# Kernel tuning notes

Measured on AMD Instinct MI355X. Metric: run time of the kernel, lower is better.

Reference implementation:

```python
import jax, jax.numpy as jnp
import numpy as np
from jax import lax

B, W_LEN, V, E, C, K, L = 8, 1000, 50000, 100, 50, 3, 18000


def setup_inputs() -> dict:
    key = jax.random.key(0)
    ks = jax.random.split(key, 7)
    return {
        "x": jax.random.randint(ks[0], (B, W_LEN), 0, V),
        "W_embed": jax.random.normal(ks[1], (V, E), dtype=jnp.float32) * 0.1,
        "conv_w": jax.random.normal(ks[2], (C, E, K), dtype=jnp.float32) * 0.08,
        "conv_b": jax.random.normal(ks[3], (C,), dtype=jnp.float32) * 0.01,
        "u_w": jax.random.normal(ks[4], (L, C), dtype=jnp.float32) * 0.1,
        "out_w": jax.random.normal(ks[5], (L, C), dtype=jnp.float32) * 0.1,
        "out_b": jax.random.normal(ks[6], (L,), dtype=jnp.float32) * 0.01,
    }


def reference(x, W_embed, conv_w, conv_b, u_w, out_w, out_b):
    # embedding lookup: (B, W, E)
    emb = W_embed[x]
    # conv1d over sequence, 'same' padding: (B, C, W)
    emb_ncw = jnp.transpose(emb, (0, 2, 1))
    H = lax.conv_general_dilated(
        emb_ncw, conv_w, window_strides=(1,), padding=[(K // 2, K // 2)],
        dimension_numbers=("NCH", "OIH", "NCH"))
    H = jnp.tanh(H + conv_b[None, :, None])
    H = jnp.transpose(H, (0, 2, 1))  # (B, W, C)
    # label-wise attention scores: (B, L, W), softmax over seq
    scores = jnp.einsum("lc,bwc->blw", u_w, H)
    attns = jax.nn.softmax(scores, axis=2)
    # attention-pooled reps: (B, L, C)
    m = jnp.einsum("blw,bwc->blc", attns, H)
    # per-label weighted dot product + bias, sigmoid: (B, L)
    out = jax.nn.sigmoid(jnp.sum(out_w[None] * m, axis=2) + out_b[None])
    return out
```

## Files before the change

### kernel.cpp

```cpp
#include <hip/hip_runtime.h>
#include <hip/hip_bf16.h>
#include <cmath>

#define AS1 __attribute__((address_space(1)))
#define AS3 __attribute__((address_space(3)))

#define B_ 8
#define W_LEN_ 1000
#define WP 1024
#define E_ 100
#define C_ 50
#define CPAD 64
#define HP 72
#define K_ 3
#define L_ 18000
#define TL 64
#define NLBLK ((L_ + TL - 1) / TL)
#define WTILE 128
#define CWT 16
#define NSLOT (K_ * (E_ / 4))

typedef __attribute__((ext_vector_type(8))) short bf16x8;
typedef __attribute__((ext_vector_type(4))) short bf16x4;
typedef __attribute__((ext_vector_type(4))) float f32x4;

static __device__ __forceinline__ void gl_lds16(const void* g, void* l) {
    __builtin_amdgcn_global_load_lds((const AS1 unsigned*)g, (AS3 unsigned*)l, 16, 0, 0);
}
static __device__ __forceinline__ float bf2f(short s) {
    return __uint_as_float(((unsigned)(unsigned short)s) << 16);
}

__global__ __launch_bounds__(256) void prep_all(
    const float* __restrict__ conv_w, const float* __restrict__ u_w,
    const float* __restrict__ out_w,
    bf16x4* __restrict__ cwTs, __hip_bfloat16* __restrict__ UO)
{
    int tid = blockIdx.x * blockDim.x + threadIdx.x;
    if (tid < NSLOT * C_) {
        int slot = tid / C_;
        int c    = tid % C_;
        int k = slot / (E_ / 4);
        int i = slot % (E_ / 4);
        bf16x4 v;
        #pragma unroll
        for (int q = 0; q < 4; q++) {
            __hip_bfloat16 h = __float2bfloat16(conv_w[((size_t)c * E_ + 4 * i + q) * K_ + k]);
            v[q] = *reinterpret_cast<short*>(&h);
        }
        cwTs[tid] = v;
    }
    if (tid < 2 * L_ * CPAD) {
        int c = tid & (CPAD - 1);
        int l = (tid >> 6) % L_;
        int m = tid / (L_ * CPAD);
        const float* src = m ? out_w : u_w;
        float v = (c < C_) ? src[(size_t)l * C_ + c] : 0.f;
        UO[tid] = __float2bfloat16(v);
    }
}

__global__ __launch_bounds__(256) void conv_kernel(
    const int* __restrict__ x,
    const float* __restrict__ W_embed,
    const bf16x4* __restrict__ cwTs,
    const float* __restrict__ conv_b,
    __hip_bfloat16* __restrict__ H)
{
    __shared__ float4 emb_s[(CWT + 2) * (E_ / 4)];
    __shared__ bf16x4 wS[NSLOT * C_];

    const int b  = blockIdx.y;
    const int w0 = blockIdx.x * CWT;
    const int tid = threadIdx.x;

    for (int i = tid; i < NSLOT * C_; i += 256) wS[i] = cwTs[i];

    for (int i = tid; i < (CWT + 2) * (E_ / 4); i += 256) {
        int row = i / (E_ / 4);
        int e4  = i % (E_ / 4);
        int ws  = w0 - 1 + row;
        float4 v = make_float4(0.f, 0.f, 0.f, 0.f);
        if ((unsigned)ws < (unsigned)W_LEN_)
            v = ((const float4*)(W_embed + (size_t)x[b * W_LEN_ + ws] * E_))[e4];
        emb_s[i] = v;
    }
    __syncthreads();

    const int c  = tid & 63;
    const int wq = tid >> 6;
    const int cc = (c < C_) ? c : 0;

    f32x4 acc[4];
    const float bias = conv_b[cc];
    #pragma unroll
    for (int j = 0; j < 4; j++) acc[j] = (f32x4){bias, 0.f, 0.f, 0.f};

    const float4* eb = &emb_s[wq * 4 * (E_ / 4)];

    #pragma unroll 5
    for (int i = 0; i < E_ / 4; i++) {
        bf16x4 kb0 = wS[i * C_ + cc];
        bf16x4 kb1 = wS[(25 + i) * C_ + cc];
        bf16x4 kb2 = wS[(50 + i) * C_ + cc];
        float4 k0 = make_float4(bf2f(kb0[0]), bf2f(kb0[1]), bf2f(kb0[2]), bf2f(kb0[3]));
        float4 k1 = make_float4(bf2f(kb1[0]), bf2f(kb1[1]), bf2f(kb1[2]), bf2f(kb1[3]));
        float4 k2 = make_float4(bf2f(kb2[0]), bf2f(kb2[1]), bf2f(kb2[2]), bf2f(kb2[3]));
        float4 e0 = eb[i],       e1 = eb[25 + i],  e2 = eb[50 + i];
        float4 e3 = eb[75 + i],  e4 = eb[100 + i], e5 = eb[125 + i];
        acc[0].x += e0.x*k0.x + e1.x*k1.x + e2.x*k2.x;
        acc[0].y += e0.y*k0.y + e1.y*k1.y + e2.y*k2.y;
        acc[0].z += e0.z*k0.z + e1.z*k1.z + e2.z*k2.z;
        acc[0].w += e0.w*k0.w + e1.w*k1.w + e2.w*k2.w;
        acc[1].x += e1.x*k0.x + e2.x*k1.x + e3.x*k2.x;
        acc[1].y += e1.y*k0.y + e2.y*k1.y + e3.y*k2.y;
        acc[1].z += e1.z*k0.z + e2.z*k1.z + e3.z*k2.z;
        acc[1].w += e1.w*k0.w + e2.w*k1.w + e3.w*k2.w;
        acc[2].x += e2.x*k0.x + e3.x*k1.x + e4.x*k2.x;
        acc[2].y += e2.y*k0.y + e3.y*k1.y + e4.y*k2.y;
        acc[2].z += e2.z*k0.z + e3.z*k1.z + e4.z*k2.z;
        acc[2].w += e2.w*k0.w + e3.w*k1.w + e4.w*k2.w;
        acc[3].x += e3.x*k0.x + e4.x*k1.x + e5.x*k2.x;
        acc[3].y += e3.y*k0.y + e4.y*k1.y + e5.y*k2.y;
        acc[3].z += e3.z*k0.z + e4.z*k1.z + e5.z*k2.z;
        acc[3].w += e3.w*k0.w + e4.w*k1.w + e5.w*k2.w;
    }

    #pragma unroll
    for (int j = 0; j < 4; j++) {
        int w = w0 + wq * 4 + j;
        float v = 0.f;
        if (c < C_ && w < W_LEN_)
            v = tanhf((acc[j].x + acc[j].z) + (acc[j].y + acc[j].w));
        __hip_bfloat16* row = H + ((size_t)b * WP + w) * HP;
        row[c] = __float2bfloat16(v);
        if (c < HP - 64) row[64 + c] = __float2bfloat16(0.f);
    }
}

__global__ __launch_bounds__(256) void attn_kernel(
    const __hip_bfloat16* __restrict__ H,
    const __hip_bfloat16* __restrict__ UO,
    const float* __restrict__ out_b,
    float* __restrict__ out)
{
    __shared__ __hip_bfloat16 Hs[2][WTILE * HP];
    __shared__ float2 red[2][TL];

    const int b  = blockIdx.y;
    const int l0 = blockIdx.x * TL;
    const int tid  = threadIdx.x;
    const int lane = tid & 63;
    const int wid  = tid >> 6;
    const int mi = wid & 1, ni = wid >> 1;
    const int col = lane & 15, quad = lane >> 4;

    bf16x8 Uf[2][2], Of[2][2];
    #pragma unroll
    for (int mt = 0; mt < 2; mt++) {
        int l = l0 + mi * 32 + mt * 16 + col;
        if (l >= L_) l = L_ - 1;
        const __hip_bfloat16* up = UO + (size_t)l * CPAD + quad * 8;
        const __hip_bfloat16* op = up + (size_t)L_ * CPAD;
        #pragma unroll
        for (int st = 0; st < 2; st++) {
            Uf[mt][st] = *(const bf16x8*)(up + st * 32);
            Of[mt][st] = *(const bf16x8*)(op + st * 32);
        }
    }

    f32x4 lsum[2] = {{0.f,0.f,0.f,0.f},{0.f,0.f,0.f,0.f}};
    f32x4 num [2] = {{0.f,0.f,0.f,0.f},{0.f,0.f,0.f,0.f}};
    const f32x4 zero = {0.f, 0.f, 0.f, 0.f};

    const __hip_bfloat16* Hb = H + (size_t)b * WP * HP;

    #define STAGE(buf, tile)                                                        \
    {                                                                               \
        const char* g = (const char*)(Hb + (size_t)(tile) * WTILE * HP);            \
        char* l = (char*)&Hs[buf][0];                                               \
        gl_lds16(g + tid * 16,          l + tid * 16);                              \
        gl_lds16(g + (tid + 256) * 16,  l + (tid + 256) * 16);                      \
        gl_lds16(g + (tid + 512) * 16,  l + (tid + 512) * 16);                      \
        gl_lds16(g + (tid + 768) * 16,  l + (tid + 768) * 16);                      \
        if (tid < 128)                                                              \
            gl_lds16(g + (tid + 1024) * 16, l + (tid + 1024) * 16);                 \
    }

    STAGE(0, 0)

    #pragma unroll 1
    for (int t = 0; t < WP / WTILE; t++) {
        const int cur = t & 1;
        __syncthreads();

        if (t + 1 < WP / WTILE)
            STAGE(cur ^ 1, t + 1)

        #pragma unroll
        for (int half = 0; half < 2; half++) {
            const __hip_bfloat16* Hc = &Hs[cur][half * 64 * HP];

            bf16x8 Bc[2][2];
            #pragma unroll
            for (int nt = 0; nt < 2; nt++)
                #pragma unroll
                for (int st = 0; st < 2; st++)
                    Bc[nt][st] = *(const bf16x8*)(&Hc[(ni * 32 + nt * 16 + col) * HP
                                                      + quad * 8 + st * 32]);

            #pragma unroll
            for (int nt = 0; nt < 2; nt++) {
                #pragma unroll
                for (int mt = 0; mt < 2; mt++) {
                    __builtin_amdgcn_s_setprio(1);
                    f32x4 S = __builtin_amdgcn_mfma_f32_16x16x32_bf16(Uf[mt][0], Bc[nt][0], zero, 0, 0, 0);
                    S       = __builtin_amdgcn_mfma_f32_16x16x32_bf16(Uf[mt][1], Bc[nt][1], S,    0, 0, 0);
                    f32x4 T = __builtin_amdgcn_mfma_f32_16x16x32_bf16(Of[mt][0], Bc[nt][0], zero, 0, 0, 0);
                    T       = __builtin_amdgcn_mfma_f32_16x16x32_bf16(Of[mt][1], Bc[nt][1], T,    0, 0, 0);
                    __builtin_amdgcn_s_setprio(0);
                    #pragma unroll
                    for (int r = 0; r < 4; r++) {
                        float p = __expf(S[r]);
                        lsum[mt][r] += p;
                        num [mt][r] += p * T[r];
                    }
                }
            }
        }
    }

    #pragma unroll
    for (int mt = 0; mt < 2; mt++) {
        #pragma unroll
        for (int r = 0; r < 4; r++) {
            float ls = lsum[mt][r], nm = num[mt][r];
            #pragma unroll
            for (int d = 1; d < 16; d <<= 1) {
                ls += __shfl_xor(ls, d, 64);
                nm += __shfl_xor(nm, d, 64);
            }
            if (col == 0)
                red[ni][mi * 32 + mt * 16 + quad * 4 + r] = make_float2(ls, nm);
        }
    }
    __syncthreads();

    if (tid < TL) {
        int l = l0 + tid;
        if (l < L_) {
            float2 p0 = red[0][tid], p1 = red[1][tid];
            float z = (p0.y + p1.y) / (p0.x + p1.x - (float)(WP - W_LEN_)) + out_b[l];
            out[(size_t)b * L_ + l] = 1.f / (1.f + __expf(-z));
        }
    }
}

extern "C" void kernel_launch(void* const* d_in, const int* in_sizes, int n_in,
                              void* d_out, int out_size, void* d_ws, size_t ws_size,
                              hipStream_t stream) {
    const int*   x       = (const int*)  d_in[0];
    const float* W_embed = (const float*)d_in[1];
    const float* conv_w  = (const float*)d_in[2];
    const float* conv_b  = (const float*)d_in[3];
    const float* u_w     = (const float*)d_in[4];
    const float* out_w   = (const float*)d_in[5];
    const float* out_b   = (const float*)d_in[6];
    float* out = (float*)d_out;

    char* ws = (char*)d_ws;
    __hip_bfloat16* H  = (__hip_bfloat16*)ws;
    __hip_bfloat16* UO = (__hip_bfloat16*)(ws + 1179648);
    bf16x4*       cwTs = (bf16x4*)(ws + 1179648 + 4608000);

    {
        const int total = 2 * L_ * CPAD;
        prep_all<<<dim3((total + 255) / 256), 256, 0, stream>>>(conv_w, u_w, out_w, cwTs, UO);
    }
    {
        dim3 grid(WP / CWT, B_);
        conv_kernel<<<grid, 256, 0, stream>>>(x, W_embed, cwTs, conv_b, H);
    }
    {
        dim3 grid(NLBLK, B_);
        attn_kernel<<<grid, 256, 0, stream>>>(H, UO, out_b, out);
    }
}
```

Measured before the change: 149.7 us.

## Load H fragments directly from global into registers instead of LDS staging

Removes the double-buffered LDS staging of H tiles (global_load_lds plus per-tile barriers) in the attention kernel. Each wave now reads its MFMA B-fragments straight from global memory, with a one-step register prefetch of the next 64-row slice. This drops the __syncthreads calls and the LDS traffic, but waves that share H rows now fetch them separately from global or L2, and the 16-byte strided loads may coalesce less well.

```diff
diff --git a/kernel.cpp b/kernel.cpp
--- a/kernel.cpp
+++ b/kernel.cpp
@@ -16,7 +16,6 @@
 #define L_ 18000
 #define TL 64
 #define NLBLK ((L_ + TL - 1) / TL)
-#define WTILE 128
 #define CWT 16
 #define NSLOT (K_ * (E_ / 4))
 
@@ -24,9 +23,6 @@
 typedef __attribute__((ext_vector_type(4))) short bf16x4;
 typedef __attribute__((ext_vector_type(4))) float f32x4;
 
-static __device__ __forceinline__ void gl_lds16(const void* g, void* l) {
-    __builtin_amdgcn_global_load_lds((const AS1 unsigned*)g, (AS3 unsigned*)l, 16, 0, 0);
-}
 static __device__ __forceinline__ float bf2f(short s) {
     return __uint_as_float(((unsigned)(unsigned short)s) << 16);
 }
@@ -144,7 +140,6 @@
     const float* __restrict__ out_b,
     float* __restrict__ out)
 {
-    __shared__ __hip_bfloat16 Hs[2][WTILE * HP];
     __shared__ float2 red[2][TL];
 
     const int b  = blockIdx.y;
@@ -173,61 +168,53 @@
     f32x4 num [2] = {{0.f,0.f,0.f,0.f},{0.f,0.f,0.f,0.f}};
     const f32x4 zero = {0.f, 0.f, 0.f, 0.f};
 
-    const __hip_bfloat16* Hb = H + (size_t)b * WP * HP;
-
-    #define STAGE(buf, tile)                                                        \
-    {                                                                               \
-        const char* g = (const char*)(Hb + (size_t)(tile) * WTILE * HP);            \
-        char* l = (char*)&Hs[buf][0];                                               \
-        gl_lds16(g + tid * 16,          l + tid * 16);                              \
-        gl_lds16(g + (tid + 256) * 16,  l + (tid + 256) * 16);                      \
-        gl_lds16(g + (tid + 512) * 16,  l + (tid + 512) * 16);                      \
-        gl_lds16(g + (tid + 768) * 16,  l + (tid + 768) * 16);                      \
-        if (tid < 128)                                                              \
-            gl_lds16(g + (tid + 1024) * 16, l + (tid + 1024) * 16);                 \
-    }
-
-    STAGE(0, 0)
+    const char* gB = (const char*)(H + (size_t)b * WP * HP)
+                   + ((size_t)(ni * 32 + col) * HP + quad * 8) * 2;
+
+    bf16x8 Bc[2][2];
+    #pragma unroll
+    for (int nt = 0; nt < 2; nt++)
+        #pragma unroll
+        for (int st = 0; st < 2; st++)
+            Bc[nt][st] = *(const bf16x8*)(gB + nt * (16 * HP * 2) + st * 64);
 
     #pragma unroll 1
-    for (int t = 0; t < WP / WTILE; t++) {
-        const int cur = t & 1;
-        __syncthreads();
-
-        if (t + 1 < WP / WTILE)
-            STAGE(cur ^ 1, t + 1)
-
-        #pragma unroll
-        for (int half = 0; half < 2; half++) {
-            const __hip_bfloat16* Hc = &Hs[cur][half * 64 * HP];
-
-            bf16x8 Bc[2][2];
+    for (int wt = 0; wt < WP; wt += 64) {
+        bf16x8 Bn[2][2];
+        if (wt + 64 < WP) {
+            const char* gN = gB + 64 * HP * 2;
             #pragma unroll
             for (int nt = 0; nt < 2; nt++)
                 #pragma unroll
                 for (int st = 0; st < 2; st++)
-                    Bc[nt][st] = *(const bf16x8*)(&Hc[(ni * 32 + nt * 16 + col) * HP
-                                                      + quad * 8 + st * 32]);
-
-            #pragma unroll
-            for (int nt = 0; nt < 2; nt++) {
+                    Bn[nt][st] = *(const bf16x8*)(gN + nt * (16 * HP * 2) + st * 64);
+        }
+        gB += 64 * HP * 2;
+
+        #pragma unroll
+        for (int nt = 0; nt < 2; nt++) {
+            #pragma unroll
+            for (int mt = 0; mt < 2; mt++) {
+                __builtin_amdgcn_s_setprio(1);
+                f32x4 S = __builtin_amdgcn_mfma_f32_16x16x32_bf16(Uf[mt][0], Bc[nt][0], zero, 0, 0, 0);
+                S       = __builtin_amdgcn_mfma_f32_16x16x32_bf16(Uf[mt][1], Bc[nt][1], S,    0, 0, 0);
+                f32x4 T = __builtin_amdgcn_mfma_f32_16x16x32_bf16(Of[mt][0], Bc[nt][0], zero, 0, 0, 0);
+                T       = __builtin_amdgcn_mfma_f32_16x16x32_bf16(Of[mt][1], Bc[nt][1], T,    0, 0, 0);
+                __builtin_amdgcn_s_setprio(0);
                 #pragma unroll
-                for (int mt = 0; mt < 2; mt++) {
-                    __builtin_amdgcn_s_setprio(1);
-                    f32x4 S = __builtin_amdgcn_mfma_f32_16x16x32_bf16(Uf[mt][0], Bc[nt][0], zero, 0, 0, 0);
-                    S       = __builtin_amdgcn_mfma_f32_16x16x32_bf16(Uf[mt][1], Bc[nt][1], S,    0, 0, 0);
-                    f32x4 T = __builtin_amdgcn_mfma_f32_16x16x32_bf16(Of[mt][0], Bc[nt][0], zero, 0, 0, 0);
-                    T       = __builtin_amdgcn_mfma_f32_16x16x32_bf16(Of[mt][1], Bc[nt][1], T,    0, 0, 0);
-                    __builtin_amdgcn_s_setprio(0);
-                    #pragma unroll
-                    for (int r = 0; r < 4; r++) {
-                        float p = __expf(S[r]);
-                        lsum[mt][r] += p;
-                        num [mt][r] += p * T[r];
-                    }
+                for (int r = 0; r < 4; r++) {
+                    float p = __expf(S[r]);
+                    lsum[mt][r] += p;
+                    num [mt][r] += p * T[r];
                 }
             }
         }
+
+        #pragma unroll
+        for (int nt = 0; nt < 2; nt++)
+            #pragma unroll
+            for (int st = 0; st < 2; st++)
+                Bc[nt][st] = Bn[nt][st];
     }
 
     #pragma unroll
```

After: 148.9 us. No clear change (-0.5%).
